# Kernel optimization log

Measured on AMD Instinct MI355X. Metric: run time of the kernel, lower is better.

The kernel has to match this reference:

```python
import jax, jax.numpy as jnp
import numpy as np

NUM_Q = 4
BETA = 0.25
TEMP = 0.1
EPS = 1e-12


def setup_inputs() -> dict:
    key = jax.random.key(0)
    k1, k2, k3, k4 = jax.random.split(key, 4)
    N, D, NE, K = 32768, 256, 256, 4096
    return {
        "x": jax.random.normal(k1, (N, D), dtype=jnp.float32),
        "codebooks": jax.random.normal(k2, (NUM_Q, NE, D), dtype=jnp.float32) * 0.02,
        "pair_idx1": jax.random.randint(k3, (K,), 0, N),
        "pair_idx2": jax.random.randint(k4, (K,), 0, N),
    }


def _quantize(residual, codebook):
    # squared L2 cdist: ||r||^2 - 2 r.e + ||e||^2  -> [N, n_e]
    d2 = (jnp.sum(residual * residual, axis=1, keepdims=True)
          - 2.0 * residual @ codebook.T
          + jnp.sum(codebook * codebook, axis=1))
    idx = jnp.argmin(d2, axis=1)                      # [N]
    q = codebook[idx]                                 # gather [N, D]
    sg = jax.lax.stop_gradient
    loss = jnp.mean((sg(q) - residual) ** 2) + BETA * jnp.mean((q - sg(residual)) ** 2)
    x_res = residual + sg(q - residual)               # straight-through
    return x_res, loss, idx


def _outer_contrastive(feat, i1, i2):
    # L2-normalize rows (torch F.normalize, eps clamp)
    xn = feat * jax.lax.rsqrt(jnp.sum(feat * feat, axis=1, keepdims=True) + EPS)
    pos = jnp.sum(xn[i1] * xn[i2], axis=1) / TEMP     # [K]
    sim = (xn[i1] @ xn.T) / TEMP                      # [K, N]
    # CE with positive at sim[:, i2]; excluded-positive column equals pos,
    # so logsumexp over [pos, negatives] == logsumexp over the full row.
    return jnp.mean(jax.nn.logsumexp(sim, axis=1) - pos)


def reference(x, codebooks, pair_idx1, pair_idx2):
    residual = x
    x_q = jnp.zeros_like(x)
    vq_losses, outer_losses, all_idx = [], [], []
    for q in range(NUM_Q):
        outer_losses.append(_outer_contrastive(residual, pair_idx1, pair_idx2))
        x_res, loss, idx = _quantize(residual, codebooks[q])
        residual = residual - x_res
        x_q = x_q + x_res
        vq_losses.append(loss)
        all_idx.append(idx)
    mean_loss = jnp.mean(jnp.stack(vq_losses))
    return (x_q, mean_loss, jnp.stack(outer_losses), jnp.stack(all_idx, axis=-1))
```

## Files before the change

kernel.cpp:

```cpp
#include <hip/hip_runtime.h>

#define N_ROWS 32768
#define DIM    256
#define NE     256
#define KP     4096
#define NQ     4
#define ND     8388608
#define RESCORE_MARGIN 2e-4f

typedef short short8 __attribute__((ext_vector_type(8)));
typedef unsigned short ushort8v __attribute__((ext_vector_type(8)));
typedef float f32x4  __attribute__((ext_vector_type(4)));

__device__ inline float bf2f(unsigned short u) {
  return __uint_as_float(((unsigned)u) << 16);
}
__device__ inline unsigned short f2bf(float f) {
  unsigned u = __float_as_uint(f);
  u += 0x7fffu + ((u >> 16) & 1u);
  return (unsigned short)(u >> 16);
}
__device__ inline float fexp2(float x) { return __builtin_amdgcn_exp2f(x); }

__device__ inline size_t chunkIdx(int row, int j) {
  return (size_t)(((row >> 4) * 8 + (j >> 2)) * 64 + ((j & 3) << 4) + (row & 15));
}

__global__ __launch_bounds__(256) void prep0_kernel(
    const float* __restrict__ x,
    unsigned short* __restrict__ Xnp, float* __restrict__ rnorm,
    unsigned short* __restrict__ rHp, unsigned short* __restrict__ rLp) {
  const int tid = threadIdx.x, wave = tid >> 6, lane = tid & 63;
  const int half = lane >> 5, j = lane & 31;
  const int row = blockIdx.x * 8 + wave * 2 + half;
  const float4* xr = (const float4*)(x + (size_t)row * DIM + j * 8);
  float4 v0 = xr[0], v1 = xr[1];
  float vv[8] = {v0.x, v0.y, v0.z, v0.w, v1.x, v1.y, v1.z, v1.w};
  float ss = 0.f;
#pragma unroll
  for (int i = 0; i < 8; ++i) ss += vv[i] * vv[i];
#pragma unroll
  for (int m = 1; m < 32; m <<= 1) ss += __shfl_xor(ss, m, 64);
  if (j == 0) rnorm[row] = ss;
  const float sc = rsqrtf(ss + 1e-12f);
  ushort8v h, l, xn;
#pragma unroll
  for (int i = 0; i < 8; ++i) {
    h[i] = f2bf(vv[i]); l[i] = f2bf(vv[i] - bf2f(h[i])); xn[i] = f2bf(vv[i] * sc);
  }
  const size_t c = chunkIdx(row, j) * 8;
  *(ushort8v*)(rHp + c) = h;
  *(ushort8v*)(rLp + c) = l;
  *(ushort8v*)(Xnp + c) = xn;
}

__global__ __launch_bounds__(256) void cbnorm_kernel(
    const float* __restrict__ cb, float* __restrict__ cbn) {
  const int wave = threadIdx.x >> 6, lane = threadIdx.x & 63;
  const int e = blockIdx.x * 4 + wave;
  float4 v = ((const float4*)(cb + (size_t)e * DIM))[lane];
  float ss = v.x * v.x + v.y * v.y + v.z * v.z + v.w * v.w;
#pragma unroll
  for (int m = 1; m < 64; m <<= 1) ss += __shfl_xor(ss, m, 64);
  if (lane == 0) cbn[e] = ss;
}

__global__ __launch_bounds__(256) void cbsplit_kernel(
    const float* __restrict__ cb, unsigned short* __restrict__ cbHp,
    unsigned short* __restrict__ cbLp) {
  const int p = blockIdx.x * 256 + threadIdx.x;
  const int stage = p >> 13, ps = p & 8191;
  const int l16 = ps & 15, quad = (ps >> 4) & 3, kf = (ps >> 6) & 7, et = ps >> 9;
  const int e = et * 16 + l16, k0 = kf * 32 + quad * 8;
  const float* src = cb + ((size_t)(stage * NE + e)) * DIM + k0;
  float4 v0 = ((const float4*)src)[0], v1 = ((const float4*)src)[1];
  float vv[8] = {v0.x, v0.y, v0.z, v0.w, v1.x, v1.y, v1.z, v1.w};
  ushort8v h, l;
#pragma unroll
  for (int i = 0; i < 8; ++i) {
    h[i] = f2bf(vv[i]); l[i] = f2bf(vv[i] - bf2f(h[i]));
  }
  *(ushort8v*)(cbHp + (size_t)p * 8) = h;
  *(ushort8v*)(cbLp + (size_t)p * 8) = l;
}

__global__ __launch_bounds__(256) void gather_pos_kernel(
    const unsigned short* __restrict__ Xnp, const int* __restrict__ i1,
    const int* __restrict__ i2, unsigned short* __restrict__ Qgp,
    float* __restrict__ pos, float* __restrict__ ssum) {
  if (blockIdx.x < 16) ssum[blockIdx.x * 256 + threadIdx.x] = 0.0f;
  const int wave = threadIdx.x >> 6, lane = threadIdx.x & 63;
  const int k = blockIdx.x * 4 + wave;
  const int a = i1[k], b = i2[k];
  const int j2 = lane >> 1, off = (lane & 1) * 4;
  ushort4 va = *(const ushort4*)(Xnp + chunkIdx(a, j2) * 8 + off);
  ushort4 vb = *(const ushort4*)(Xnp + chunkIdx(b, j2) * 8 + off);
  *(ushort4*)(Qgp + chunkIdx(k, j2) * 8 + off) = va;
  float d = bf2f(va.x) * bf2f(vb.x) + bf2f(va.y) * bf2f(vb.y) +
            bf2f(va.z) * bf2f(vb.z) + bf2f(va.w) * bf2f(vb.w);
#pragma unroll
  for (int m = 1; m < 64; m <<= 1) d += __shfl_xor(d, m, 64);
  if (lane == 0) pos[k] = d * 10.0f;
}

__global__ __launch_bounds__(256, 2) void sim_lse_kernel(
    const unsigned short* __restrict__ Qgp, const unsigned short* __restrict__ Xnp,
    float* __restrict__ s_sum) {
  __shared__ unsigned short ldsB[4096];
  const int tid  = threadIdx.x;
  const int lane = tid & 63;
  const int wave = tid >> 6;
  const int quad = lane >> 4;
  const int l16  = lane & 15;

  const int fid = blockIdx.y * 32 + blockIdx.x;
  const int xcd = fid & 7;
  const int sl  = fid >> 3;
  const int bx  = sl & 31;
  const int by  = xcd * 8 + (sl >> 5);

  const int qt0  = bx * 8 + wave * 2;
  const int qbase = bx * 128 + wave * 32;

  short8 a[2][8];
#pragma unroll
  for (int t = 0; t < 2; ++t)
#pragma unroll
    for (int f = 0; f < 8; ++f)
      a[t][f] = *(const short8*)(Qgp + ((size_t)(((qt0 + t) * 8 + f) * 64 + lane)) * 8);

  float s[2][4] = {};
  const float C1 = 14.4269504088896341f;
  const unsigned short* bsrc = Xnp + (size_t)(by * 32) * 4096;

  auto stageB = [&](int g) {
    const unsigned short* src = bsrc + (size_t)g * 4096 + wave * 1024 + lane * 8;
#pragma unroll
    for (int p = 0; p < 2; ++p)
      __builtin_amdgcn_global_load_lds(
          (const __attribute__((address_space(1))) unsigned int*)(src + p * 512),
          (__attribute__((address_space(3))) unsigned int*)(&ldsB[wave * 1024 + p * 512]),
          16, 0, 0);
  };

  stageB(0);
  for (int g = 0; g < 32; ++g) {
    asm volatile("s_waitcnt vmcnt(0)" ::: "memory");
    __builtin_amdgcn_s_barrier();
    __builtin_amdgcn_sched_barrier(0);
    short8 b[8];
#pragma unroll
    for (int f = 0; f < 8; ++f)
      b[f] = *(const short8*)(&ldsB[f * 512 + lane * 8]);
    asm volatile("s_waitcnt lgkmcnt(0)" ::: "memory");
    __builtin_amdgcn_s_barrier();
    __builtin_amdgcn_sched_barrier(0);
    if (g + 1 < 32) stageB(g + 1);

    f32x4 acc0[2] = {{0.f, 0.f, 0.f, 0.f}, {0.f, 0.f, 0.f, 0.f}};
    f32x4 acc1[2] = {{0.f, 0.f, 0.f, 0.f}, {0.f, 0.f, 0.f, 0.f}};
#pragma unroll
    for (int f = 0; f < 4; ++f)
#pragma unroll
      for (int t = 0; t < 2; ++t) {
        acc0[t] = __builtin_amdgcn_mfma_f32_16x16x32_bf16(a[t][f], b[f], acc0[t], 0, 0, 0);
        acc1[t] = __builtin_amdgcn_mfma_f32_16x16x32_bf16(a[t][f + 4], b[f + 4], acc1[t], 0, 0, 0);
      }
#pragma unroll
    for (int t = 0; t < 2; ++t) {
      f32x4 m = acc0[t] + acc1[t];
#pragma unroll
      for (int i = 0; i < 4; ++i)
        s[t][i] += fexp2(fmaf(m[i], C1, -C1));
    }
  }
#pragma unroll
  for (int m = 1; m < 16; m <<= 1)
#pragma unroll
    for (int t = 0; t < 2; ++t)
#pragma unroll
      for (int i = 0; i < 4; ++i) s[t][i] += __shfl_xor(s[t][i], m, 64);
  if (l16 == 0) {
#pragma unroll
    for (int t = 0; t < 2; ++t)
#pragma unroll
      for (int i = 0; i < 4; ++i)
        atomicAdd(&s_sum[qbase + t * 16 + quad * 4 + i], s[t][i]);
  }
}

__global__ __launch_bounds__(256) void lse_final_kernel(
    const float* __restrict__ s_sum, const float* __restrict__ pos,
    float* __restrict__ acc, int stage) {
  const int t = threadIdx.x;
  const int k = blockIdx.x * 256 + t;
  float v = 10.0f + __logf(s_sum[k]) - pos[k];
#pragma unroll
  for (int m = 1; m < 64; m <<= 1) v += __shfl_xor(v, m, 64);
  __shared__ float red[4];
  if ((t & 63) == 0) red[t >> 6] = v;
  __syncthreads();
  if (t == 0) atomicAdd(&acc[4 + stage], red[0] + red[1] + red[2] + red[3]);
}

__global__ __launch_bounds__(256, 2) void argmin_update_kernel(
    const float* __restrict__ xin, float* __restrict__ resid,
    const float* __restrict__ cb,
    const unsigned short* __restrict__ cbHp, const unsigned short* __restrict__ cbLp,
    const float* __restrict__ cbn, float* __restrict__ rnorm,
    unsigned short* rHp, unsigned short* rLp,
    float* __restrict__ xq, float* __restrict__ idxf, float* __restrict__ acc,
    unsigned short* __restrict__ Xnp, int stage) {
  __shared__ float sV1[4][32];
  __shared__ float sV2[4][32];
  __shared__ int   sIx[4][32];
  __shared__ int   sIdx[32];
  __shared__ int   sFlag[32];
  __shared__ float sred[4];
  const int tid  = threadIdx.x;
  const int lane = tid & 63;
  const int wave = tid >> 6;
  const int quad = lane >> 4;
  const int l16  = lane & 15;
  const int rbase = blockIdx.x * 32;
  const int t0 = blockIdx.x * 2;
  const float* __restrict__ src = (stage == 0) ? xin : resid;

  f32x4 acc4[2][4];
#pragma unroll
  for (int rt = 0; rt < 2; ++rt)
#pragma unroll
    for (int ct = 0; ct < 4; ++ct) acc4[rt][ct] = (f32x4){0.f, 0.f, 0.f, 0.f};

  auto loadA = [&](int kf, short8 (&aH)[2], short8 (&aL)[2]) {
#pragma unroll
    for (int rt = 0; rt < 2; ++rt) {
      const size_t off = ((size_t)(((t0 + rt) * 8 + kf) * 64 + lane)) * 8;
      aH[rt] = *(const short8*)(rHp + off);
      aL[rt] = *(const short8*)(rLp + off);
    }
  };
  auto loadBc = [&](int kf, short8 (&bH)[4], short8 (&bL)[4]) {
#pragma unroll
    for (int ct = 0; ct < 4; ++ct) {
      const size_t boff = ((size_t)(((wave * 4 + ct) * 8 + kf) * 64 + lane)) * 8;
      bH[ct] = *(const short8*)(cbHp + boff);
      bL[ct] = *(const short8*)(cbLp + boff);
    }
  };
  auto computeK = [&](short8 (&aH)[2], short8 (&aL)[2], short8 (&bH)[4],
                      short8 (&bL)[4]) {
#pragma unroll
    for (int ct = 0; ct < 4; ++ct)
#pragma unroll
      for (int rt = 0; rt < 2; ++rt) {
        acc4[rt][ct] = __builtin_amdgcn_mfma_f32_16x16x32_bf16(aL[rt], bH[ct], acc4[rt][ct], 0, 0, 0);
        acc4[rt][ct] = __builtin_amdgcn_mfma_f32_16x16x32_bf16(aH[rt], bL[ct], acc4[rt][ct], 0, 0, 0);
        acc4[rt][ct] = __builtin_amdgcn_mfma_f32_16x16x32_bf16(aH[rt], bH[ct], acc4[rt][ct], 0, 0, 0);
      }
  };

  short8 aH0[2], aL0[2], bH0[4], bL0[4], aH1[2], aL1[2], bH1[4], bL1[4];
  loadA(0, aH0, aL0); loadBc(0, bH0, bL0);
  for (int kf = 0; kf < 8; kf += 2) {
    loadA(kf + 1, aH1, aL1); loadBc(kf + 1, bH1, bL1);
    computeK(aH0, aL0, bH0, bL0);
    if (kf + 2 < 8) { loadA(kf + 2, aH0, aL0); loadBc(kf + 2, bH0, bL0); }
    computeK(aH1, aL1, bH1, bL1);
  }

  float cbe[4];
#pragma unroll
  for (int ct = 0; ct < 4; ++ct) cbe[ct] = cbn[(wave * 4 + ct) * 16 + l16];
#pragma unroll
  for (int rt = 0; rt < 2; ++rt) {
    float b1[4], b2[4]; int e1[4];
#pragma unroll
    for (int i = 0; i < 4; ++i) { b1[i] = 3.4e38f; b2[i] = 3.4e38f; e1[i] = 0; }
#pragma unroll
    for (int ct = 0; ct < 4; ++ct) {
      const int e = (wave * 4 + ct) * 16 + l16;
#pragma unroll
      for (int i = 0; i < 4; ++i) {
        const float v = fmaf(-2.0f, acc4[rt][ct][i], cbe[ct]);
        if (v < b1[i]) { b2[i] = b1[i]; b1[i] = v; e1[i] = e; }
        else if (v < b2[i]) b2[i] = v;
      }
    }
#pragma unroll
    for (int m = 1; m < 16; m <<= 1) {
#pragma unroll
      for (int i = 0; i < 4; ++i) {
        const float o1 = __shfl_xor(b1[i], m, 64);
        const float o2 = __shfl_xor(b2[i], m, 64);
        const int   oe = __shfl_xor(e1[i], m, 64);
        if (o1 < b1[i] || (o1 == b1[i] && oe < e1[i])) {
          b2[i] = fminf(b1[i], o2); b1[i] = o1; e1[i] = oe;
        } else {
          b2[i] = fminf(b2[i], o1);
        }
      }
    }
    if (l16 == 0) {
#pragma unroll
      for (int i = 0; i < 4; ++i) {
        const int r = rt * 16 + quad * 4 + i;
        sV1[wave][r] = b1[i]; sV2[wave][r] = b2[i]; sIx[wave][r] = e1[i];
      }
    }
  }
  __syncthreads();
  if (tid < 32) {
    float v1 = 3.4e38f, v2 = 3.4e38f; int ix = 0;
#pragma unroll
    for (int w = 0; w < 4; ++w) {
      const float a1 = sV1[w][tid], a2 = sV2[w][tid];
      const int ae = sIx[w][tid];
      if (a1 < v1) { v2 = fminf(v1, a2); v1 = a1; ix = ae; }
      else { v2 = fminf(v2, fminf(a1, a2)); }
    }
    sIdx[tid] = ix;
    sFlag[tid] = (v2 - v1 < RESCORE_MARGIN) ? 1 : 0;
  }
  __syncthreads();

  for (int rr = 0; rr < 8; ++rr) {
    const int r = wave * 8 + rr;
    if (sFlag[r]) {
      const int row = rbase + r;
      const float* rrow = src + (size_t)row * DIM;
      float d[4] = {0.f, 0.f, 0.f, 0.f};
      for (int kb = 0; kb < 64; ++kb) {
        const float4 rv = ((const float4*)rrow)[kb];
#pragma unroll
        for (int j = 0; j < 4; ++j) {
          const float4 cv = ((const float4*)(cb + (size_t)(lane + 64 * j) * DIM))[kb];
          d[j] = fmaf(rv.x, cv.x, d[j]);
          d[j] = fmaf(rv.y, cv.y, d[j]);
          d[j] = fmaf(rv.z, cv.z, d[j]);
          d[j] = fmaf(rv.w, cv.w, d[j]);
        }
      }
      const float rn = rnorm[row];
      float bv = 3.4e38f; int be = 0;
#pragma unroll
      for (int j = 0; j < 4; ++j) {
        const int e = lane + 64 * j;
        const float v = (rn - 2.0f * d[j]) + cbn[e];
        if (v < bv) { bv = v; be = e; }
      }
#pragma unroll
      for (int m = 1; m < 64; m <<= 1) {
        const float vo = __shfl_xor(bv, m, 64);
        const int   eo = __shfl_xor(be, m, 64);
        if (vo < bv || (vo == bv && eo < be)) { bv = vo; be = eo; }
      }
      if (lane == 0) sIdx[r] = be;
    }
  }
  __syncthreads();

  const int half = lane >> 5, j = lane & 31;
  float msum = 0.0f;
  for (int i = 0; i < 4; ++i) {
    const int rr = i * 8 + wave * 2 + half;
    const int row = rbase + rr;
    const int e = sIdx[rr];
    const float4* rp = (const float4*)(src + (size_t)row * DIM + j * 8);
    float4 r0 = rp[0], r1 = rp[1];
    const float4* qp = (const float4*)(cb + (size_t)e * DIM + j * 8);
    float4 q0 = qp[0], q1 = qp[1];
    float nr[8] = {r0.x - q0.x, r0.y - q0.y, r0.z - q0.z, r0.w - q0.w,
                   r1.x - q1.x, r1.y - q1.y, r1.z - q1.z, r1.w - q1.w};
    float ss = 0.f;
#pragma unroll
    for (int u = 0; u < 8; ++u) ss += nr[u] * nr[u];
    if (stage == 3) {
      const float4* xr = (const float4*)(xin + (size_t)row * DIM + j * 8);
      float4 x0 = xr[0], x1 = xr[1];
      float4* xp = (float4*)(xq + (size_t)row * DIM + j * 8);
      xp[0] = (float4){x0.x - nr[0], x0.y - nr[1], x0.z - nr[2], x0.w - nr[3]};
      xp[1] = (float4){x1.x - nr[4], x1.y - nr[5], x1.z - nr[6], x1.w - nr[7]};
    }
#pragma unroll
    for (int m = 1; m < 32; m <<= 1) ss += __shfl_xor(ss, m, 64);
    if (stage < 3) {
      float4* rw = (float4*)(resid + (size_t)row * DIM + j * 8);
      rw[0] = (float4){nr[0], nr[1], nr[2], nr[3]};
      rw[1] = (float4){nr[4], nr[5], nr[6], nr[7]};
      const float sc = rsqrtf(ss + 1e-12f);
      ushort8v h, l, xn;
#pragma unroll
      for (int u = 0; u < 8; ++u) {
        h[u] = f2bf(nr[u]); l[u] = f2bf(nr[u] - bf2f(h[u])); xn[u] = f2bf(nr[u] * sc);
      }
      const size_t c = chunkIdx(row, j) * 8;
      *(ushort8v*)(rHp + c) = h;
      *(ushort8v*)(rLp + c) = l;
      *(ushort8v*)(Xnp + c) = xn;
      if (j == 0) rnorm[row] = ss;
    }
    if (j == 0) {
      idxf[(size_t)row * NQ + stage] = (float)e;
      msum += ss;
    }
  }
  msum += __shfl_xor(msum, 32, 64);
  if (lane == 0) sred[wave] = msum;
  __syncthreads();
  if (tid == 0) atomicAdd(&acc[0], sred[0] + sred[1] + sred[2] + sred[3]);
}

__global__ void finalize_kernel(const float* __restrict__ acc, float* __restrict__ out) {
  const int t = threadIdx.x;
  if (t == 0) out[ND] = acc[0] * (1.25f / (4.0f * (float)ND));
  if (t < 4) out[ND + 1 + t] = acc[4 + t] * (1.0f / (float)KP);
}

extern "C" void kernel_launch(void* const* d_in, const int* in_sizes, int n_in,
                              void* d_out, int out_size, void* d_ws, size_t ws_size,
                              hipStream_t stream) {
  const float* x         = (const float*)d_in[0];
  const float* codebooks = (const float*)d_in[1];
  const int*   i1        = (const int*)d_in[2];
  const int*   i2        = (const int*)d_in[3];
  float* out = (float*)d_out;
  float* out_xq   = out;
  float* out_idxf = out + ND + 1 + NQ;

  char* w = (char*)d_ws;
  float*          resid = (float*)w;          w += (size_t)N_ROWS * DIM * 4;
  unsigned short* Xnp   = (unsigned short*)w; w += (size_t)N_ROWS * DIM * 2;
  unsigned short* rHp   = (unsigned short*)w; w += (size_t)N_ROWS * DIM * 2;
  unsigned short* rLp   = (unsigned short*)w; w += (size_t)N_ROWS * DIM * 2;
  float*          rnorm = (float*)w;          w += (size_t)N_ROWS * 4;
  unsigned short* Qgp   = (unsigned short*)w; w += (size_t)KP * DIM * 2;
  float*          pos   = (float*)w;          w += (size_t)KP * 4;
  float*          ssum  = (float*)w;          w += (size_t)KP * 4;
  float*          cbn   = (float*)w;          w += (size_t)NQ * NE * 4;
  unsigned short* cbHp  = (unsigned short*)w; w += (size_t)NQ * NE * DIM * 2;
  unsigned short* cbLp  = (unsigned short*)w; w += (size_t)NQ * NE * DIM * 2;
  float*          acc   = (float*)w;          w += 32;

  prep0_kernel<<<4096, 256, 0, stream>>>(x, Xnp, rnorm, rHp, rLp);
  cbnorm_kernel<<<256, 256, 0, stream>>>(codebooks, cbn);
  cbsplit_kernel<<<128, 256, 0, stream>>>(codebooks, cbHp, cbLp);
  hipMemsetAsync(acc, 0, 32, stream);
  for (int q = 0; q < NQ; ++q) {
    const float* cb = codebooks + (size_t)q * NE * DIM;
    gather_pos_kernel<<<1024, 256, 0, stream>>>(Xnp, i1, i2, Qgp, pos, ssum);
    sim_lse_kernel<<<dim3(32, 64), 256, 0, stream>>>(Qgp, Xnp, ssum);
    lse_final_kernel<<<16, 256, 0, stream>>>(ssum, pos, acc, q);
    argmin_update_kernel<<<1024, 256, 0, stream>>>(
        x, resid, cb, cbHp + (size_t)q * NE * DIM, cbLp + (size_t)q * NE * DIM,
        cbn + q * NE, rnorm, rHp, rLp, out_xq, out_idxf, acc, Xnp, q);
  }
  finalize_kernel<<<1, 64, 0, stream>>>(acc, out);
}
```

Baseline: 617.0 us.

## Split argmin from residual update and coalesce packed-fragment writes via LDS transpose

Separates the argmin/update kernel into an argmin-only kernel that writes indices to a scratch buffer, plus a new update kernel. The update kernel, like prep0, reads whole rows per wave and stages them in LDS so that each packed bf16 hi/lo/normalized chunk is written contiguously. The aim is fully coalesced stores and lower register pressure in the MFMA argmin kernel. The cost is an extra launch per stage and an extra round trip of indices through global memory, which reuses the Qgp buffer as scratch.

```diff
diff --git a/kernel.cpp b/kernel.cpp
--- a/kernel.cpp
+++ b/kernel.cpp
@@ -26,32 +26,46 @@
   return (size_t)(((row >> 4) * 8 + (j >> 2)) * 64 + ((j & 3) << 4) + (row & 15));
 }
 
+
 __global__ __launch_bounds__(256) void prep0_kernel(
     const float* __restrict__ x,
     unsigned short* __restrict__ Xnp, float* __restrict__ rnorm,
     unsigned short* __restrict__ rHp, unsigned short* __restrict__ rLp) {
+  __shared__ float ldsNr[16 * 260];
+  __shared__ float ssl[16];
   const int tid = threadIdx.x, wave = tid >> 6, lane = tid & 63;
-  const int half = lane >> 5, j = lane & 31;
-  const int row = blockIdx.x * 8 + wave * 2 + half;
-  const float4* xr = (const float4*)(x + (size_t)row * DIM + j * 8);
-  float4 v0 = xr[0], v1 = xr[1];
-  float vv[8] = {v0.x, v0.y, v0.z, v0.w, v1.x, v1.y, v1.z, v1.w};
-  float ss = 0.f;
-#pragma unroll
-  for (int i = 0; i < 8; ++i) ss += vv[i] * vv[i];
-#pragma unroll
-  for (int m = 1; m < 32; m <<= 1) ss += __shfl_xor(ss, m, 64);
-  if (j == 0) rnorm[row] = ss;
-  const float sc = rsqrtf(ss + 1e-12f);
-  ushort8v h, l, xn;
-#pragma unroll
-  for (int i = 0; i < 8; ++i) {
-    h[i] = f2bf(vv[i]); l[i] = f2bf(vv[i] - bf2f(h[i])); xn[i] = f2bf(vv[i] * sc);
-  }
-  const size_t c = chunkIdx(row, j) * 8;
-  *(ushort8v*)(rHp + c) = h;
-  *(ushort8v*)(rLp + c) = l;
-  *(ushort8v*)(Xnp + c) = xn;
+  const int t = blockIdx.x;
+#pragma unroll
+  for (int rr = 0; rr < 4; ++rr) {
+    const int rl = wave * 4 + rr;
+    const int row = t * 16 + rl;
+    float4 v = ((const float4*)(x + (size_t)row * DIM))[lane];
+    float ss = v.x * v.x + v.y * v.y + v.z * v.z + v.w * v.w;
+#pragma unroll
+    for (int m = 1; m < 64; m <<= 1) ss += __shfl_xor(ss, m, 64);
+    *(float4*)(&ldsNr[rl * 260 + lane * 4]) = v;
+    if (lane == 0) { ssl[rl] = ss; rnorm[row] = ss; }
+  }
+  __syncthreads();
+  const int l16 = lane & 15, quad = lane >> 4;
+  const float sc = rsqrtf(ssl[l16] + 1e-12f);
+#pragma unroll
+  for (int ff = 0; ff < 2; ++ff) {
+    const int f = wave * 2 + ff;
+    const float* p = &ldsNr[l16 * 260 + f * 32 + quad * 8];
+    float4 u0 = *(const float4*)(p);
+    float4 u1 = *(const float4*)(p + 4);
+    float vv[8] = {u0.x, u0.y, u0.z, u0.w, u1.x, u1.y, u1.z, u1.w};
+    ushort8v h, l, xn;
+#pragma unroll
+    for (int u = 0; u < 8; ++u) {
+      h[u] = f2bf(vv[u]); l[u] = f2bf(vv[u] - bf2f(h[u])); xn[u] = f2bf(vv[u] * sc);
+    }
+    const size_t c = ((size_t)(t * 8 + f) * 64 + lane) * 8;
+    *(ushort8v*)(rHp + c) = h;
+    *(ushort8v*)(rLp + c) = l;
+    *(ushort8v*)(Xnp + c) = xn;
+  }
 }
 
 __global__ __launch_bounds__(256) void cbnorm_kernel(
@@ -203,20 +217,18 @@
   if (t == 0) atomicAdd(&acc[4 + stage], red[0] + red[1] + red[2] + red[3]);
 }
 
-__global__ __launch_bounds__(256, 2) void argmin_update_kernel(
-    const float* __restrict__ xin, float* __restrict__ resid,
+__global__ __launch_bounds__(256, 2) void argmin_kernel(
+    const float* __restrict__ xin, const float* __restrict__ resid,
     const float* __restrict__ cb,
     const unsigned short* __restrict__ cbHp, const unsigned short* __restrict__ cbLp,
-    const float* __restrict__ cbn, float* __restrict__ rnorm,
-    unsigned short* rHp, unsigned short* rLp,
-    float* __restrict__ xq, float* __restrict__ idxf, float* __restrict__ acc,
-    unsigned short* __restrict__ Xnp, int stage) {
+    const float* __restrict__ cbn, const float* __restrict__ rnorm,
+    const unsigned short* __restrict__ rHp, const unsigned short* __restrict__ rLp,
+    int* __restrict__ outIdx, int stage) {
   __shared__ float sV1[4][32];
   __shared__ float sV2[4][32];
   __shared__ int   sIx[4][32];
   __shared__ int   sIdx[32];
   __shared__ int   sFlag[32];
-  __shared__ float sred[4];
   const int tid  = threadIdx.x;
   const int lane = tid & 63;
   const int wave = tid >> 6;
@@ -359,56 +371,75 @@
     }
   }
   __syncthreads();
-
-  const int half = lane >> 5, j = lane & 31;
-  float msum = 0.0f;
-  for (int i = 0; i < 4; ++i) {
-    const int rr = i * 8 + wave * 2 + half;
-    const int row = rbase + rr;
-    const int e = sIdx[rr];
-    const float4* rp = (const float4*)(src + (size_t)row * DIM + j * 8);
-    float4 r0 = rp[0], r1 = rp[1];
-    const float4* qp = (const float4*)(cb + (size_t)e * DIM + j * 8);
-    float4 q0 = qp[0], q1 = qp[1];
-    float nr[8] = {r0.x - q0.x, r0.y - q0.y, r0.z - q0.z, r0.w - q0.w,
-                   r1.x - q1.x, r1.y - q1.y, r1.z - q1.z, r1.w - q1.w};
-    float ss = 0.f;
-#pragma unroll
-    for (int u = 0; u < 8; ++u) ss += nr[u] * nr[u];
-    if (stage == 3) {
-      const float4* xr = (const float4*)(xin + (size_t)row * DIM + j * 8);
-      float4 x0 = xr[0], x1 = xr[1];
-      float4* xp = (float4*)(xq + (size_t)row * DIM + j * 8);
-      xp[0] = (float4){x0.x - nr[0], x0.y - nr[1], x0.z - nr[2], x0.w - nr[3]};
-      xp[1] = (float4){x1.x - nr[4], x1.y - nr[5], x1.z - nr[6], x1.w - nr[7]};
-    }
-#pragma unroll
-    for (int m = 1; m < 32; m <<= 1) ss += __shfl_xor(ss, m, 64);
+  if (tid < 32) outIdx[rbase + tid] = sIdx[tid];
+}
+
+__global__ __launch_bounds__(256) void update_kernel(
+    const float* __restrict__ xin, float* __restrict__ resid,
+    const float* __restrict__ cb, const int* __restrict__ idx,
+    float* __restrict__ rnorm,
+    unsigned short* __restrict__ rHp, unsigned short* __restrict__ rLp,
+    unsigned short* __restrict__ Xnp,
+    float* __restrict__ xq, float* __restrict__ idxf, float* __restrict__ acc,
+    int stage) {
+  __shared__ float ldsNr[16 * 260];
+  __shared__ float ssl[16];
+  __shared__ float sred[4];
+  const int tid = threadIdx.x, wave = tid >> 6, lane = tid & 63;
+  const int t = blockIdx.x;
+  const float* __restrict__ src = (stage == 0) ? xin : resid;
+
+  float msum = 0.f;
+#pragma unroll
+  for (int rr = 0; rr < 4; ++rr) {
+    const int rl = wave * 4 + rr;
+    const int row = t * 16 + rl;
+    const int e = idx[row];
+    float4 v = ((const float4*)(src + (size_t)row * DIM))[lane];
+    float4 c = ((const float4*)(cb + (size_t)e * DIM))[lane];
+    float4 nr = {v.x - c.x, v.y - c.y, v.z - c.z, v.w - c.w};
+    float ss = nr.x * nr.x + nr.y * nr.y + nr.z * nr.z + nr.w * nr.w;
+#pragma unroll
+    for (int m = 1; m < 64; m <<= 1) ss += __shfl_xor(ss, m, 64);
     if (stage < 3) {
-      float4* rw = (float4*)(resid + (size_t)row * DIM + j * 8);
-      rw[0] = (float4){nr[0], nr[1], nr[2], nr[3]};
-      rw[1] = (float4){nr[4], nr[5], nr[6], nr[7]};
-      const float sc = rsqrtf(ss + 1e-12f);
+      ((float4*)(resid + (size_t)row * DIM))[lane] = nr;
+      *(float4*)(&ldsNr[rl * 260 + lane * 4]) = nr;
+      if (lane == 0) { ssl[rl] = ss; rnorm[row] = ss; }
+    } else {
+      float4 xv = ((const float4*)(xin + (size_t)row * DIM))[lane];
+      ((float4*)(xq + (size_t)row * DIM))[lane] =
+          (float4){xv.x - nr.x, xv.y - nr.y, xv.z - nr.z, xv.w - nr.w};
+    }
+    if (lane == 0) {
+      idxf[(size_t)row * NQ + stage] = (float)e;
+      msum += ss;
+    }
+  }
+  if (lane == 0) sred[wave] = msum;
+  __syncthreads();
+  if (tid == 0) atomicAdd(&acc[0], sred[0] + sred[1] + sred[2] + sred[3]);
+
+  if (stage < 3) {
+    const int l16 = lane & 15, quad = lane >> 4;
+    const float sc = rsqrtf(ssl[l16] + 1e-12f);
+#pragma unroll
+    for (int ff = 0; ff < 2; ++ff) {
+      const int f = wave * 2 + ff;
+      const float* p = &ldsNr[l16 * 260 + f * 32 + quad * 8];
+      float4 u0 = *(const float4*)(p);
+      float4 u1 = *(const float4*)(p + 4);
+      float vv[8] = {u0.x, u0.y, u0.z, u0.w, u1.x, u1.y, u1.z, u1.w};
       ushort8v h, l, xn;
 #pragma unroll
       for (int u = 0; u < 8; ++u) {
-        h[u] = f2bf(nr[u]); l[u] = f2bf(nr[u] - bf2f(h[u])); xn[u] = f2bf(nr[u] * sc);
-      }
-      const size_t c = chunkIdx(row, j) * 8;
+        h[u] = f2bf(vv[u]); l[u] = f2bf(vv[u] - bf2f(h[u])); xn[u] = f2bf(vv[u] * sc);
+      }
+      const size_t c = ((size_t)(t * 8 + f) * 64 + lane) * 8;
       *(ushort8v*)(rHp + c) = h;
       *(ushort8v*)(rLp + c) = l;
       *(ushort8v*)(Xnp + c) = xn;
-      if (j == 0) rnorm[row] = ss;
-    }
-    if (j == 0) {
-      idxf[(size_t)row * NQ + stage] = (float)e;
-      msum += ss;
-    }
-  }
-  msum += __shfl_xor(msum, 32, 64);
-  if (lane == 0) sred[wave] = msum;
-  __syncthreads();
-  if (tid == 0) atomicAdd(&acc[0], sred[0] + sred[1] + sred[2] + sred[3]);
+    }
+  }
 }
 
 __global__ void finalize_kernel(const float* __restrict__ acc, float* __restrict__ out) {
@@ -441,8 +472,9 @@
   unsigned short* cbHp  = (unsigned short*)w; w += (size_t)NQ * NE * DIM * 2;
   unsigned short* cbLp  = (unsigned short*)w; w += (size_t)NQ * NE * DIM * 2;
   float*          acc   = (float*)w;          w += 32;
-
-  prep0_kernel<<<4096, 256, 0, stream>>>(x, Xnp, rnorm, rHp, rLp);
+  int* sidx = (int*)Qgp;
+
+  prep0_kernel<<<2048, 256, 0, stream>>>(x, Xnp, rnorm, rHp, rLp);
   cbnorm_kernel<<<256, 256, 0, stream>>>(codebooks, cbn);
   cbsplit_kernel<<<128, 256, 0, stream>>>(codebooks, cbHp, cbLp);
   hipMemsetAsync(acc, 0, 32, stream);
@@ -451,9 +483,11 @@
     gather_pos_kernel<<<1024, 256, 0, stream>>>(Xnp, i1, i2, Qgp, pos, ssum);
     sim_lse_kernel<<<dim3(32, 64), 256, 0, stream>>>(Qgp, Xnp, ssum);
     lse_final_kernel<<<16, 256, 0, stream>>>(ssum, pos, acc, q);
-    argmin_update_kernel<<<1024, 256, 0, stream>>>(
+    argmin_kernel<<<1024, 256, 0, stream>>>(
         x, resid, cb, cbHp + (size_t)q * NE * DIM, cbLp + (size_t)q * NE * DIM,
-        cbn + q * NE, rnorm, rHp, rLp, out_xq, out_idxf, acc, Xnp, q);
+        cbn + q * NE, rnorm, rHp, rLp, sidx, q);
+    update_kernel<<<2048, 256, 0, stream>>>(
+        x, resid, cb, sidx, rnorm, rHp, rLp, Xnp, out_xq, out_idxf, acc, q);
   }
   finalize_kernel<<<1, 64, 0, stream>>>(acc, out);
 }
```

New measurement: 703.3 us. +14.0%, slower.
